# Kernel optimization log

Measured on AMD Instinct MI355X. Metric: run time of the kernel, lower is better.

Reference implementation:

```python
import jax, jax.numpy as jnp
import numpy as np

H = 2048            # hidden_size
INTER = 8192        # intermediate_size
E = 16              # num_experts
V = 32000           # vocab_size
I = INTER // E      # per-expert intermediate (tp_size=1) = 512
N = 4096            # num_tokens
BASE_ROUTING_SCALE = 10.0


def setup_inputs() -> dict:
    key = jax.random.key(0)
    ks = jax.random.split(key, 6)
    x = jax.random.normal(ks[0], (N, H), dtype=jnp.float32)
    token_ids = jax.random.randint(ks[1], (N,), 0, V)
    mu = jax.random.normal(ks[2], (N, H), dtype=jnp.float32)
    # kaiming-uniform-ish scaled params
    gate_up_proj = jax.random.normal(ks[3], (E, H, 2 * I), dtype=jnp.float32) * (1.0 / np.sqrt(H))
    down_proj = jax.random.normal(ks[4], (E, I, H), dtype=jnp.float32) * (1.0 / np.sqrt(I))
    # mu_router initialized to zeros in the module; use small random so routing is actually mu-biased
    mu_router_w = jax.random.normal(ks[5], (E, H), dtype=jnp.float32) * 0.02
    return {"x": x, "token_ids": token_ids, "mu": mu,
            "gate_up_proj": gate_up_proj, "down_proj": down_proj,
            "mu_router_w": mu_router_w}


def reference(x, token_ids, mu, gate_up_proj, down_proj, mu_router_w):
    # --- routing: expert = token_id % E, biased by mu logits ---
    base = jnp.clip(token_ids, 0, V - 1) % E              # [N]
    logits = (jax.nn.one_hot(base, E, dtype=jnp.float32) * BASE_ROUTING_SCALE
              + mu @ mu_router_w.T)                       # [N, E]
    expert_ids = jnp.argmax(logits, axis=-1)              # [N]

    Iloc = gate_up_proj.shape[-1] // 2

    # --- grouped expert SwiGLU MLP: scan over experts, mask-combine outputs ---
    def step(acc, inp):
        wg, wd, e = inp
        gu = x @ wg                                       # [N, 2I]
        h = jax.nn.silu(gu[:, :Iloc]) * gu[:, Iloc:]      # [N, I]
        o = h @ wd                                        # [N, H]
        acc = acc + jnp.where((expert_ids == e)[:, None], o, 0.0)
        return acc, None

    out0 = jnp.zeros_like(x)
    out, _ = jax.lax.scan(step, out0, (gate_up_proj, down_proj, jnp.arange(E)))
    return out
```

## Files before the change

### kernel.cpp

```cpp
#include <hip/hip_runtime.h>
#include <hip/hip_bf16.h>

#define NT 4096
#define HD 2048
#define NE 16
#define ID 512
#define TWO_I 1024
#define PITCH 72
#define MAXITEMS 47

typedef __attribute__((ext_vector_type(8))) short bf16x8_t;
typedef __attribute__((ext_vector_type(4))) float f32x4_t;

__device__ __forceinline__ unsigned short f2bf(float f) {
  union { float f; unsigned int u; } v; v.f = f;
  unsigned int r = v.u + 0x7fffu + ((v.u >> 16) & 1u);
  return (unsigned short)(r >> 16);
}
__device__ __forceinline__ unsigned pk2(unsigned short a, unsigned short b) {
  return (unsigned)a | ((unsigned)b << 16);
}
__device__ __forceinline__ void gl_lds16(const void* g, void* l) {
  __builtin_amdgcn_global_load_lds(
      (const __attribute__((address_space(1))) unsigned int*)g,
      (__attribute__((address_space(3))) unsigned int*)l, 16, 0, 0);
}

__global__ __launch_bounds__(256) void k_prep_gu(const float* __restrict__ gup,
                                                 unsigned short* __restrict__ wgb) {
  int e = blockIdx.y, k0 = blockIdx.x * 32;
  int t = threadIdx.x;
  int cb = t >> 4, c = (t & 15) * 4;
  const float* src = gup + ((size_t)e * HD + k0) * TWO_I + t * 4;
  unsigned short* dst = wgb + (((size_t)e * 16 + cb) * HD + k0) * 64 + c;
#pragma unroll 4
  for (int j = 0; j < 32; ++j) {
    float4 v = *(const float4*)src; src += TWO_I;
    uint2 p; p.x = pk2(f2bf(v.x), f2bf(v.y)); p.y = pk2(f2bf(v.z), f2bf(v.w));
    *(uint2*)dst = p; dst += 64;
  }
}
__global__ __launch_bounds__(256) void k_prep_dn(const float* __restrict__ dwn,
                                                 unsigned short* __restrict__ wdb) {
  int e = blockIdx.y, k0 = blockIdx.x * 32;
  int t = threadIdx.x;
  int cb = t >> 3, c = (t & 7) * 8;
  const float* src = dwn + ((size_t)e * ID + k0) * HD + t * 8;
  unsigned short* dst = wdb + (((size_t)e * 32 + cb) * ID + k0) * 64 + c;
#pragma unroll 4
  for (int j = 0; j < 32; ++j) {
    float4 v0 = *(const float4*)src;
    float4 v1 = *(const float4*)(src + 4); src += HD;
    uint4 p;
    p.x = pk2(f2bf(v0.x), f2bf(v0.y)); p.y = pk2(f2bf(v0.z), f2bf(v0.w));
    p.z = pk2(f2bf(v1.x), f2bf(v1.y)); p.w = pk2(f2bf(v1.z), f2bf(v1.w));
    *(uint4*)dst = p; dst += 64;
  }
}

__global__ void k_cast_x(const float* __restrict__ x, unsigned short* __restrict__ xb) {
  size_t i = ((size_t)blockIdx.x * 256 + threadIdx.x) * 8;
  float4 a = *(const float4*)(x + i);
  float4 b = *(const float4*)(x + i + 4);
  uint4 pk;
  pk.x = pk2(f2bf(a.x), f2bf(a.y)); pk.y = pk2(f2bf(a.z), f2bf(a.w));
  pk.z = pk2(f2bf(b.x), f2bf(b.y)); pk.w = pk2(f2bf(b.z), f2bf(b.w));
  *(uint4*)(xb + i) = pk;
}

__global__ void k_route(const float* __restrict__ mu, const int* __restrict__ tok,
                        const float* __restrict__ wr, int* __restrict__ eid) {
  int t = blockIdx.x;
  int tid = threadIdx.x;
  float p[NE];
#pragma unroll
  for (int e = 0; e < NE; ++e) p[e] = 0.f;
  const float* m = mu + (size_t)t * HD;
  for (int h = tid; h < HD; h += 256) {
    float mv = m[h];
#pragma unroll
    for (int e = 0; e < NE; ++e) p[e] += mv * wr[e * HD + h];
  }
#pragma unroll
  for (int e = 0; e < NE; ++e) {
    float v = p[e];
#pragma unroll
    for (int s = 32; s; s >>= 1) v += __shfl_xor(v, s, 64);
    p[e] = v;
  }
  __shared__ float red[4][NE];
  int lane = tid & 63, wv = tid >> 6;
  if (lane == 0) {
#pragma unroll
    for (int e = 0; e < NE; ++e) red[wv][e] = p[e];
  }
  __syncthreads();
  if (tid == 0) {
    int tk = tok[t];
    if (tk < 0) tk = 0;
    if (tk > 31999) tk = 31999;
    int base = tk & 15;
    float best = -3.0e38f; int bi = 0;
    for (int e = 0; e < NE; ++e) {
      float v = red[0][e] + red[1][e] + red[2][e] + red[3][e];
      if (e == base) v += 10.0f;
      if (v > best) { best = v; bi = e; }
    }
    eid[t] = bi;
  }
}

__global__ void k_init(int* counts, int* cursors) {
  int i = threadIdx.x;
  if (i < NE) { counts[i] = 0; cursors[i] = 0; }
}
__global__ void k_hist(const int* __restrict__ eid, int* __restrict__ counts) {
  int t = blockIdx.x * 256 + threadIdx.x;
  if (t < NT) atomicAdd(&counts[eid[t]], 1);
}
__global__ void k_scan(const int* __restrict__ counts, int* __restrict__ offsets,
                       int* __restrict__ cursors, int* __restrict__ wk) {
  if (threadIdx.x == 0) {
    int s = 0;
    for (int e = 0; e < NE; ++e) { offsets[e] = s; cursors[e] = s; s += counts[e]; }
    offsets[NE] = s;
    int n = 0;
    for (int e = 0; e < NE; ++e) {
      int tiles = (counts[e] + 127) >> 7;
      for (int m = 0; m < tiles; ++m) { wk[n++] = e | (m << 8); }
    }
    wk[MAXITEMS] = n;
  }
}
__global__ void k_scatter(const int* __restrict__ eid, int* __restrict__ cursors,
                          int* __restrict__ tlist) {
  int t = blockIdx.x * 256 + threadIdx.x;
  if (t < NT) {
    int e = eid[t];
    int pos = atomicAdd(&cursors[e], 1);
    tlist[pos] = t;
  }
}

__global__ __launch_bounds__(256, 2) void k_gemm1(
    const unsigned short* __restrict__ xb, const unsigned short* __restrict__ wgb,
    const int* __restrict__ offsets, const int* __restrict__ tlist,
    const int* __restrict__ wk, unsigned short* __restrict__ hbuf) {
  int item = blockIdx.y;
  if (item >= wk[MAXITEMS]) return;
  int w = wk[item];
  int e = w & 255, tb = (w >> 8) * 128;
  int off = offsets[e], cnt = offsets[e + 1] - off;
  int cx = blockIdx.x;
  int c0 = cx * 64;

  __shared__ unsigned short Bb[2][2][64 * 64];
  __shared__ unsigned short Pb[2][128 * PITCH];
  __shared__ int ltok[128];

  int tid = threadIdx.x, lane = tid & 63, wv = tid >> 6;
  if (tid < 128) { int r = tb + tid; if (r > cnt - 1) r = cnt - 1; ltok[tid] = tlist[off + r]; }
  __syncthreads();

  int lr = lane & 15, hi = lane >> 4, mb = wv * 32;
  const unsigned short* aRow0 = xb + (size_t)ltok[mb + lr] * HD + hi * 8;
  const unsigned short* aRow1 = xb + (size_t)ltok[mb + 16 + lr] * HD + hi * 8;

  const unsigned short* gS0;
  const unsigned short* gS1;
  const unsigned short* uS0;
  const unsigned short* uS1;
  {
    const unsigned short* gbase = wgb + ((size_t)(e * 16 + cx) * HD) * 64;
    const unsigned short* ubase = wgb + ((size_t)(e * 16 + 8 + cx) * HD) * 64;
    int lo = lane * 8;
    gS0 = gbase + (wv * 16) * 64 + lo;      gS1 = gbase + (wv * 16 + 8) * 64 + lo;
    uS0 = ubase + (wv * 16) * 64 + lo;      uS1 = ubase + (wv * 16 + 8) * 64 + lo;
  }

#define STAGEB(BUF) do { \
  gl_lds16(gS0, &Bb[BUF][0][(wv * 16) * 64]);     gS0 += 4096; \
  gl_lds16(gS1, &Bb[BUF][0][(wv * 16 + 8) * 64]); gS1 += 4096; \
  gl_lds16(uS0, &Bb[BUF][1][(wv * 16) * 64]);     uS0 += 4096; \
  gl_lds16(uS1, &Bb[BUF][1][(wv * 16 + 8) * 64]); uS1 += 4096; \
} while (0)

  bf16x8_t A0[4], A1[4];
#define LOADA(SET, KT) do { \
  SET[0] = *(const bf16x8_t*)(aRow0 + (KT) * 64); \
  SET[1] = *(const bf16x8_t*)(aRow0 + (KT) * 64 + 32); \
  SET[2] = *(const bf16x8_t*)(aRow1 + (KT) * 64); \
  SET[3] = *(const bf16x8_t*)(aRow1 + (KT) * 64 + 32); \
} while (0)

#define TRANSP(BUF) do { \
  int T_ = lane >> 5, c2_ = (lane & 31) * 2; \
  const unsigned short* b_ = &Bb[BUF][T_][(wv * 16) * 64 + c2_]; \
  unsigned v_[16]; \
  _Pragma("unroll") for (int j = 0; j < 16; ++j) v_[j] = *(const unsigned*)(b_ + j * 64); \
  uint4 lo0_, lo1_, hi0_, hi1_; \
  lo0_.x = (v_[0] & 0xffffu) | (v_[1] << 16);  lo0_.y = (v_[2] & 0xffffu) | (v_[3] << 16); \
  lo0_.z = (v_[4] & 0xffffu) | (v_[5] << 16);  lo0_.w = (v_[6] & 0xffffu) | (v_[7] << 16); \
  lo1_.x = (v_[8] & 0xffffu) | (v_[9] << 16);  lo1_.y = (v_[10] & 0xffffu) | (v_[11] << 16); \
  lo1_.z = (v_[12] & 0xffffu) | (v_[13] << 16); lo1_.w = (v_[14] & 0xffffu) | (v_[15] << 16); \
  hi0_.x = (v_[0] >> 16) | (v_[1] & 0xffff0000u);  hi0_.y = (v_[2] >> 16) | (v_[3] & 0xffff0000u); \
  hi0_.z = (v_[4] >> 16) | (v_[5] & 0xffff0000u);  hi0_.w = (v_[6] >> 16) | (v_[7] & 0xffff0000u); \
  hi1_.x = (v_[8] >> 16) | (v_[9] & 0xffff0000u);  hi1_.y = (v_[10] >> 16) | (v_[11] & 0xffff0000u); \
  hi1_.z = (v_[12] >> 16) | (v_[13] & 0xffff0000u); hi1_.w = (v_[14] >> 16) | (v_[15] & 0xffff0000u); \
  unsigned short* p0_ = &Pb[BUF][(T_ * 64 + c2_) * PITCH + wv * 16]; \
  *(uint4*)p0_ = lo0_; *(uint4*)(p0_ + 8) = lo1_; \
  *(uint4*)(p0_ + PITCH) = hi0_; *(uint4*)(p0_ + PITCH + 8) = hi1_; \
} while (0)

  f32x4_t zero = {0.f, 0.f, 0.f, 0.f};
  f32x4_t accg[2][4], accu[2][4];
#pragma unroll
  for (int m = 0; m < 2; ++m)
#pragma unroll
    for (int n = 0; n < 4; ++n) { accg[m][n] = zero; accu[m][n] = zero; }

#define MFMA_PH(BUF, SET) do { \
  __builtin_amdgcn_s_setprio(1); \
  _Pragma("unroll") for (int kk = 0; kk < 2; ++kk) { \
    int klo = kk * 32 + hi * 8; \
    bf16x8_t a0 = SET[kk], a1 = SET[2 + kk]; \
    _Pragma("unroll") for (int n = 0; n < 4; ++n) { \
      bf16x8_t bg = *(bf16x8_t*)&Pb[BUF][(n * 16 + lr) * PITCH + klo]; \
      bf16x8_t bu = *(bf16x8_t*)&Pb[BUF][(64 + n * 16 + lr) * PITCH + klo]; \
      accg[0][n] = __builtin_amdgcn_mfma_f32_16x16x32_bf16(a0, bg, accg[0][n], 0, 0, 0); \
      accu[0][n] = __builtin_amdgcn_mfma_f32_16x16x32_bf16(a0, bu, accu[0][n], 0, 0, 0); \
      accg[1][n] = __builtin_amdgcn_mfma_f32_16x16x32_bf16(a1, bg, accg[1][n], 0, 0, 0); \
      accu[1][n] = __builtin_amdgcn_mfma_f32_16x16x32_bf16(a1, bu, accu[1][n], 0, 0, 0); \
    } \
  } \
  __builtin_amdgcn_s_setprio(0); \
} while (0)

#define SUBSTEP(KT, BUF, SET, VMC) do { \
  asm volatile("s_waitcnt vmcnt(" #VMC ")" ::: "memory"); \
  __builtin_amdgcn_sched_barrier(0); \
  TRANSP(BUF); \
  asm volatile("s_waitcnt lgkmcnt(0)" ::: "memory"); \
  __builtin_amdgcn_sched_barrier(0); \
  __builtin_amdgcn_s_barrier(); \
  MFMA_PH(BUF, SET); \
  if ((KT) + 2 < 32) { LOADA(SET, (KT) + 2); STAGEB(BUF); } \
} while (0)

  LOADA(A0, 0); STAGEB(0);
  LOADA(A1, 1); STAGEB(1);

  for (int kt2 = 0; kt2 < 15; ++kt2) {
    SUBSTEP(2 * kt2, 0, A0, 8);
    SUBSTEP(2 * kt2 + 1, 1, A1, 8);
  }
  SUBSTEP(30, 0, A0, 8);
  SUBSTEP(31, 1, A1, 0);

#undef SUBSTEP
#undef MFMA_PH
#undef TRANSP
#undef LOADA
#undef STAGEB

  int rq = hi * 4;
#pragma unroll
  for (int m = 0; m < 2; ++m)
#pragma unroll
    for (int n = 0; n < 4; ++n)
#pragma unroll
      for (int j = 0; j < 4; ++j) {
        int r = tb + mb + m * 16 + rq + j;
        if (r < cnt) {
          float g = accg[m][n][j], u = accu[m][n][j];
          float hv = (g / (1.f + __expf(-g))) * u;
          hbuf[(size_t)(off + r) * ID + c0 + n * 16 + lr] = f2bf(hv);
        }
      }
}

__global__ __launch_bounds__(256, 2) void k_gemm2(
    const unsigned short* __restrict__ hbuf, const unsigned short* __restrict__ wdb,
    const int* __restrict__ offsets, const int* __restrict__ tlist,
    const int* __restrict__ wk, float* __restrict__ out) {
  int item = blockIdx.y;
  if (item >= wk[MAXITEMS]) return;
  int w = wk[item];
  int e = w & 255, tb = (w >> 8) * 128;
  int off = offsets[e], cnt = offsets[e + 1] - off;
  int cx = blockIdx.x;
  int c0 = cx * 128;

  __shared__ unsigned short Bb[2][2][64 * 64];
  __shared__ unsigned short Pb[2][128 * PITCH];

  int tid = threadIdx.x, lane = tid & 63, wv = tid >> 6;
  int lr = lane & 15, hi = lane >> 4, mb = wv * 32;

  int r0 = tb + mb + lr;      if (r0 > cnt - 1) r0 = cnt - 1;
  int r1 = tb + mb + 16 + lr; if (r1 > cnt - 1) r1 = cnt - 1;
  const unsigned short* aRow0 = hbuf + (size_t)(off + r0) * ID + hi * 8;
  const unsigned short* aRow1 = hbuf + (size_t)(off + r1) * ID + hi * 8;

  const unsigned short* gS0;
  const unsigned short* gS1;
  const unsigned short* uS0;
  const unsigned short* uS1;
  {
    const unsigned short* b0 = wdb + ((size_t)(e * 32 + 2 * cx) * ID) * 64;
    const unsigned short* b1 = wdb + ((size_t)(e * 32 + 2 * cx + 1) * ID) * 64;
    int lo = lane * 8;
    gS0 = b0 + (wv * 16) * 64 + lo;  gS1 = b0 + (wv * 16 + 8) * 64 + lo;
    uS0 = b1 + (wv * 16) * 64 + lo;  uS1 = b1 + (wv * 16 + 8) * 64 + lo;
  }

#define STAGEB(BUF) do { \
  gl_lds16(gS0, &Bb[BUF][0][(wv * 16) * 64]);     gS0 += 4096; \
  gl_lds16(gS1, &Bb[BUF][0][(wv * 16 + 8) * 64]); gS1 += 4096; \
  gl_lds16(uS0, &Bb[BUF][1][(wv * 16) * 64]);     uS0 += 4096; \
  gl_lds16(uS1, &Bb[BUF][1][(wv * 16 + 8) * 64]); uS1 += 4096; \
} while (0)

  bf16x8_t A0[4], A1[4];
#define LOADA(SET, KT) do { \
  SET[0] = *(const bf16x8_t*)(aRow0 + (KT) * 64); \
  SET[1] = *(const bf16x8_t*)(aRow0 + (KT) * 64 + 32); \
  SET[2] = *(const bf16x8_t*)(aRow1 + (KT) * 64); \
  SET[3] = *(const bf16x8_t*)(aRow1 + (KT) * 64 + 32); \
} while (0)

#define TRANSP(BUF) do { \
  int T_ = lane >> 5, c2_ = (lane & 31) * 2; \
  const unsigned short* b_ = &Bb[BUF][T_][(wv * 16) * 64 + c2_]; \
  unsigned v_[16]; \
  _Pragma("unroll") for (int j = 0; j < 16; ++j) v_[j] = *(const unsigned*)(b_ + j * 64); \
  uint4 lo0_, lo1_, hi0_, hi1_; \
  lo0_.x = (v_[0] & 0xffffu) | (v_[1] << 16);  lo0_.y = (v_[2] & 0xffffu) | (v_[3] << 16); \
  lo0_.z = (v_[4] & 0xffffu) | (v_[5] << 16);  lo0_.w = (v_[6] & 0xffffu) | (v_[7] << 16); \
  lo1_.x = (v_[8] & 0xffffu) | (v_[9] << 16);  lo1_.y = (v_[10] & 0xffffu) | (v_[11] << 16); \
  lo1_.z = (v_[12] & 0xffffu) | (v_[13] << 16); lo1_.w = (v_[14] & 0xffffu) | (v_[15] << 16); \
  hi0_.x = (v_[0] >> 16) | (v_[1] & 0xffff0000u);  hi0_.y = (v_[2] >> 16) | (v_[3] & 0xffff0000u); \
  hi0_.z = (v_[4] >> 16) | (v_[5] & 0xffff0000u);  hi0_.w = (v_[6] >> 16) | (v_[7] & 0xffff0000u); \
  hi1_.x = (v_[8] >> 16) | (v_[9] & 0xffff0000u);  hi1_.y = (v_[10] >> 16) | (v_[11] & 0xffff0000u); \
  hi1_.z = (v_[12] >> 16) | (v_[13] & 0xffff0000u); hi1_.w = (v_[14] >> 16) | (v_[15] & 0xffff0000u); \
  unsigned short* p0_ = &Pb[BUF][(T_ * 64 + c2_) * PITCH + wv * 16]; \
  *(uint4*)p0_ = lo0_; *(uint4*)(p0_ + 8) = lo1_; \
  *(uint4*)(p0_ + PITCH) = hi0_; *(uint4*)(p0_ + PITCH + 8) = hi1_; \
} while (0)

  f32x4_t zero = {0.f, 0.f, 0.f, 0.f};
  f32x4_t acc[2][8];
#pragma unroll
  for (int m = 0; m < 2; ++m)
#pragma unroll
    for (int n = 0; n < 8; ++n) acc[m][n] = zero;

#define MFMA_PH(BUF, SET) do { \
  __builtin_amdgcn_s_setprio(1); \
  _Pragma("unroll") for (int kk = 0; kk < 2; ++kk) { \
    int klo = kk * 32 + hi * 8; \
    bf16x8_t a0 = SET[kk], a1 = SET[2 + kk]; \
    _Pragma("unroll") for (int n = 0; n < 8; ++n) { \
      bf16x8_t b = *(bf16x8_t*)&Pb[BUF][(n * 16 + lr) * PITCH + klo]; \
      acc[0][n] = __builtin_amdgcn_mfma_f32_16x16x32_bf16(a0, b, acc[0][n], 0, 0, 0); \
      acc[1][n] = __builtin_amdgcn_mfma_f32_16x16x32_bf16(a1, b, acc[1][n], 0, 0, 0); \
    } \
  } \
  __builtin_amdgcn_s_setprio(0); \
} while (0)

#define SUBSTEP(KT, BUF, SET, VMC) do { \
  asm volatile("s_waitcnt vmcnt(" #VMC ")" ::: "memory"); \
  __builtin_amdgcn_sched_barrier(0); \
  TRANSP(BUF); \
  asm volatile("s_waitcnt lgkmcnt(0)" ::: "memory"); \
  __builtin_amdgcn_sched_barrier(0); \
  __builtin_amdgcn_s_barrier(); \
  MFMA_PH(BUF, SET); \
  if ((KT) + 2 < 8) { LOADA(SET, (KT) + 2); STAGEB(BUF); } \
} while (0)

  LOADA(A0, 0); STAGEB(0);
  LOADA(A1, 1); STAGEB(1);

  SUBSTEP(0, 0, A0, 8);
  SUBSTEP(1, 1, A1, 8);
  SUBSTEP(2, 0, A0, 8);
  SUBSTEP(3, 1, A1, 8);
  SUBSTEP(4, 0, A0, 8);
  SUBSTEP(5, 1, A1, 8);
  SUBSTEP(6, 0, A0, 8);
  SUBSTEP(7, 1, A1, 0);

#undef SUBSTEP
#undef MFMA_PH
#undef TRANSP
#undef LOADA
#undef STAGEB

  int rq = hi * 4;
#pragma unroll
  for (int m = 0; m < 2; ++m)
#pragma unroll
    for (int n = 0; n < 8; ++n)
#pragma unroll
      for (int j = 0; j < 4; ++j) {
        int r = tb + mb + m * 16 + rq + j;
        if (r < cnt) {
          out[(size_t)tlist[off + r] * HD + c0 + n * 16 + lr] = acc[m][n][j];
        }
      }
}

extern "C" void kernel_launch(void* const* d_in, const int* in_sizes, int n_in,
                              void* d_out, int out_size, void* d_ws, size_t ws_size,
                              hipStream_t stream) {
  (void)in_sizes; (void)n_in; (void)out_size; (void)ws_size;
  const float* x   = (const float*)d_in[0];
  const int*   tok = (const int*)d_in[1];
  const float* mu  = (const float*)d_in[2];
  const float* gup = (const float*)d_in[3];
  const float* dwn = (const float*)d_in[4];
  const float* wr  = (const float*)d_in[5];
  float* out = (float*)d_out;

  char* ws = (char*)d_ws;
  int* eid     = (int*)ws;
  int* tlist   = (int*)(ws + 16384);
  int* counts  = (int*)(ws + 32768);
  int* offsets = (int*)(ws + 32896);
  int* cursors = (int*)(ws + 33024);
  int* wk      = (int*)(ws + 33152);
  unsigned short* xb   = (unsigned short*)(ws + 65536);
  unsigned short* hbuf = (unsigned short*)(ws + 65536 + 16777216);
  unsigned short* wgb  = (unsigned short*)(ws + 65536 + 16777216 + 4194304);
  unsigned short* wdb  = (unsigned short*)(ws + 65536 + 16777216 + 4194304 + 67108864);

  k_prep_gu<<<dim3(64, 16), 256, 0, stream>>>(gup, wgb);
  k_prep_dn<<<dim3(16, 16), 256, 0, stream>>>(dwn, wdb);
  k_cast_x <<<4096, 256, 0, stream>>>(x, xb);
  k_route  <<<NT, 256, 0, stream>>>(mu, tok, wr, eid);
  k_init   <<<1, 64, 0, stream>>>(counts, cursors);
  k_hist   <<<16, 256, 0, stream>>>(eid, counts);
  k_scan   <<<1, 64, 0, stream>>>(counts, offsets, cursors, wk);
  k_scatter<<<16, 256, 0, stream>>>(eid, cursors, tlist);
  k_gemm1  <<<dim3(8, MAXITEMS), 256, 0, stream>>>(xb, wgb, offsets, tlist, wk, hbuf);
  k_gemm2  <<<dim3(16, MAXITEMS), 256, 0, stream>>>(hbuf, wdb, offsets, tlist, wk, out);
}
```

Measured before the change: 234.3 us.

## Pre-transpose and XOR-swizzle weights in prep kernels; deepen GEMM pipeline to four stages

The weight prep kernels now transpose each 64x64 bf16 tile through shared memory and store it in an XOR-swizzled, MFMA-ready layout. The GEMM kernels therefore no longer run a per-iteration LDS transpose pass with its extra LDS traffic and lgkmcnt wait. Both GEMMs also move from double to quad buffering, prefetching three k-tiles ahead with four register sets for A. The cost is more LDS per block, which may limit occupancy, and a prep kernel that now synchronizes on shared memory.

```diff
diff --git a/kernel.cpp b/kernel.cpp
--- a/kernel.cpp
+++ b/kernel.cpp
@@ -6,7 +6,6 @@
 #define NE 16
 #define ID 512
 #define TWO_I 1024
-#define PITCH 72
 #define MAXITEMS 47
 
 typedef __attribute__((ext_vector_type(8))) short bf16x8_t;
@@ -28,33 +27,70 @@
 
 __global__ __launch_bounds__(256) void k_prep_gu(const float* __restrict__ gup,
                                                  unsigned short* __restrict__ wgb) {
-  int e = blockIdx.y, k0 = blockIdx.x * 32;
-  int t = threadIdx.x;
-  int cb = t >> 4, c = (t & 15) * 4;
-  const float* src = gup + ((size_t)e * HD + k0) * TWO_I + t * 4;
-  unsigned short* dst = wgb + (((size_t)e * 16 + cb) * HD + k0) * 64 + c;
-#pragma unroll 4
-  for (int j = 0; j < 32; ++j) {
-    float4 v = *(const float4*)src; src += TWO_I;
-    uint2 p; p.x = pk2(f2bf(v.x), f2bf(v.y)); p.y = pk2(f2bf(v.z), f2bf(v.w));
-    *(uint2*)dst = p; dst += 64;
+  int kt = blockIdx.x, e = blockIdx.y;
+  int K0 = kt * 64;
+  int t = threadIdx.x, w = t >> 6, lane = t & 63;
+  __shared__ unsigned short L[64][264];
+  for (int q = 0; q < 4; ++q) {
+    for (int rd = 0; rd < 16; ++rd) {
+      int row = rd * 4 + w;
+      const float* s = gup + ((size_t)e * HD + K0 + row) * TWO_I + q * 256 + lane * 4;
+      float4 v = *(const float4*)s;
+      uint2 p; p.x = pk2(f2bf(v.x), f2bf(v.y)); p.y = pk2(f2bf(v.z), f2bf(v.w));
+      *(uint2*)&L[row][lane * 4] = p;
+    }
+    __syncthreads();
+    int cbl = (t >> 5) & 3, c = (t & 31) * 2, kh = t >> 7;
+    int cb = q * 4 + cbl;
+    unsigned short* tb = wgb + (((size_t)e * 16 + cb) * 32 + kt) * 4096;
+    int cc = cbl * 64 + c;
+    for (int j = kh * 4; j < kh * 4 + 4; ++j) {
+      unsigned vv[8];
+#pragma unroll
+      for (int i = 0; i < 8; ++i) vv[i] = *(const unsigned*)&L[j * 8 + i][cc];
+      uint4 lo, hi2;
+      lo.x = (vv[0] & 0xffffu) | (vv[1] << 16);  lo.y = (vv[2] & 0xffffu) | (vv[3] << 16);
+      lo.z = (vv[4] & 0xffffu) | (vv[5] << 16);  lo.w = (vv[6] & 0xffffu) | (vv[7] << 16);
+      hi2.x = (vv[0] >> 16) | (vv[1] & 0xffff0000u);  hi2.y = (vv[2] >> 16) | (vv[3] & 0xffff0000u);
+      hi2.z = (vv[4] >> 16) | (vv[5] & 0xffff0000u);  hi2.w = (vv[6] >> 16) | (vv[7] & 0xffff0000u);
+      *(uint4*)&tb[c * 64 + ((j ^ (c & 7)) * 8)] = lo;
+      *(uint4*)&tb[(c + 1) * 64 + ((j ^ ((c + 1) & 7)) * 8)] = hi2;
+    }
+    __syncthreads();
   }
 }
 __global__ __launch_bounds__(256) void k_prep_dn(const float* __restrict__ dwn,
                                                  unsigned short* __restrict__ wdb) {
-  int e = blockIdx.y, k0 = blockIdx.x * 32;
-  int t = threadIdx.x;
-  int cb = t >> 3, c = (t & 7) * 8;
-  const float* src = dwn + ((size_t)e * ID + k0) * HD + t * 8;
-  unsigned short* dst = wdb + (((size_t)e * 32 + cb) * ID + k0) * 64 + c;
-#pragma unroll 4
-  for (int j = 0; j < 32; ++j) {
-    float4 v0 = *(const float4*)src;
-    float4 v1 = *(const float4*)(src + 4); src += HD;
-    uint4 p;
-    p.x = pk2(f2bf(v0.x), f2bf(v0.y)); p.y = pk2(f2bf(v0.z), f2bf(v0.w));
-    p.z = pk2(f2bf(v1.x), f2bf(v1.y)); p.w = pk2(f2bf(v1.z), f2bf(v1.w));
-    *(uint4*)dst = p; dst += 64;
+  int kt = blockIdx.x, e = blockIdx.y, half = blockIdx.z;
+  int K0 = kt * 64;
+  int t = threadIdx.x, w = t >> 6, lane = t & 63;
+  __shared__ unsigned short L[64][264];
+  for (int q = 0; q < 4; ++q) {
+    for (int rd = 0; rd < 16; ++rd) {
+      int row = rd * 4 + w;
+      const float* s = dwn + ((size_t)e * ID + K0 + row) * HD + half * 1024 + q * 256 + lane * 4;
+      float4 v = *(const float4*)s;
+      uint2 p; p.x = pk2(f2bf(v.x), f2bf(v.y)); p.y = pk2(f2bf(v.z), f2bf(v.w));
+      *(uint2*)&L[row][lane * 4] = p;
+    }
+    __syncthreads();
+    int cbl = (t >> 5) & 3, c = (t & 31) * 2, kh = t >> 7;
+    int cb = half * 16 + q * 4 + cbl;
+    unsigned short* tb = wdb + (((size_t)e * 32 + cb) * 8 + kt) * 4096;
+    int cc = cbl * 64 + c;
+    for (int j = kh * 4; j < kh * 4 + 4; ++j) {
+      unsigned vv[8];
+#pragma unroll
+      for (int i = 0; i < 8; ++i) vv[i] = *(const unsigned*)&L[j * 8 + i][cc];
+      uint4 lo, hi2;
+      lo.x = (vv[0] & 0xffffu) | (vv[1] << 16);  lo.y = (vv[2] & 0xffffu) | (vv[3] << 16);
+      lo.z = (vv[4] & 0xffffu) | (vv[5] << 16);  lo.w = (vv[6] & 0xffffu) | (vv[7] << 16);
+      hi2.x = (vv[0] >> 16) | (vv[1] & 0xffff0000u);  hi2.y = (vv[2] >> 16) | (vv[3] & 0xffff0000u);
+      hi2.z = (vv[4] >> 16) | (vv[5] & 0xffff0000u);  hi2.w = (vv[6] >> 16) | (vv[7] & 0xffff0000u);
+      *(uint4*)&tb[c * 64 + ((j ^ (c & 7)) * 8)] = lo;
+      *(uint4*)&tb[(c + 1) * 64 + ((j ^ ((c + 1) & 7)) * 8)] = hi2;
+    }
+    __syncthreads();
   }
 }
 
@@ -154,8 +190,7 @@
   int cx = blockIdx.x;
   int c0 = cx * 64;
 
-  __shared__ unsigned short Bb[2][2][64 * 64];
-  __shared__ unsigned short Pb[2][128 * PITCH];
+  __shared__ unsigned short Pb[4][2][4096];
   __shared__ int ltok[128];
 
   int tid = threadIdx.x, lane = tid & 63, wv = tid >> 6;
@@ -166,51 +201,23 @@
   const unsigned short* aRow0 = xb + (size_t)ltok[mb + lr] * HD + hi * 8;
   const unsigned short* aRow1 = xb + (size_t)ltok[mb + 16 + lr] * HD + hi * 8;
 
-  const unsigned short* gS0;
-  const unsigned short* gS1;
-  const unsigned short* uS0;
-  const unsigned short* uS1;
-  {
-    const unsigned short* gbase = wgb + ((size_t)(e * 16 + cx) * HD) * 64;
-    const unsigned short* ubase = wgb + ((size_t)(e * 16 + 8 + cx) * HD) * 64;
-    int lo = lane * 8;
-    gS0 = gbase + (wv * 16) * 64 + lo;      gS1 = gbase + (wv * 16 + 8) * 64 + lo;
-    uS0 = ubase + (wv * 16) * 64 + lo;      uS1 = ubase + (wv * 16 + 8) * 64 + lo;
-  }
+  int gu = wv >> 1, part = wv & 1;
+  const unsigned short* wS =
+      wgb + (((size_t)e * 16 + (gu ? 8 + cx : cx)) * 32) * 4096 + part * 2048 + lane * 8;
 
 #define STAGEB(BUF) do { \
-  gl_lds16(gS0, &Bb[BUF][0][(wv * 16) * 64]);     gS0 += 4096; \
-  gl_lds16(gS1, &Bb[BUF][0][(wv * 16 + 8) * 64]); gS1 += 4096; \
-  gl_lds16(uS0, &Bb[BUF][1][(wv * 16) * 64]);     uS0 += 4096; \
-  gl_lds16(uS1, &Bb[BUF][1][(wv * 16 + 8) * 64]); uS1 += 4096; \
-} while (0)
-
-  bf16x8_t A0[4], A1[4];
+  gl_lds16(wS,        &Pb[BUF][gu][part * 2048]); \
+  gl_lds16(wS + 512,  &Pb[BUF][gu][part * 2048 + 512]); \
+  gl_lds16(wS + 1024, &Pb[BUF][gu][part * 2048 + 1024]); \
+  gl_lds16(wS + 1536, &Pb[BUF][gu][part * 2048 + 1536]); \
+  wS += 4096; } while (0)
+
+  bf16x8_t A0[4], A1[4], A2[4], A3[4];
 #define LOADA(SET, KT) do { \
   SET[0] = *(const bf16x8_t*)(aRow0 + (KT) * 64); \
   SET[1] = *(const bf16x8_t*)(aRow0 + (KT) * 64 + 32); \
   SET[2] = *(const bf16x8_t*)(aRow1 + (KT) * 64); \
-  SET[3] = *(const bf16x8_t*)(aRow1 + (KT) * 64 + 32); \
-} while (0)
-
-#define TRANSP(BUF) do { \
-  int T_ = lane >> 5, c2_ = (lane & 31) * 2; \
-  const unsigned short* b_ = &Bb[BUF][T_][(wv * 16) * 64 + c2_]; \
-  unsigned v_[16]; \
-  _Pragma("unroll") for (int j = 0; j < 16; ++j) v_[j] = *(const unsigned*)(b_ + j * 64); \
-  uint4 lo0_, lo1_, hi0_, hi1_; \
-  lo0_.x = (v_[0] & 0xffffu) | (v_[1] << 16);  lo0_.y = (v_[2] & 0xffffu) | (v_[3] << 16); \
-  lo0_.z = (v_[4] & 0xffffu) | (v_[5] << 16);  lo0_.w = (v_[6] & 0xffffu) | (v_[7] << 16); \
-  lo1_.x = (v_[8] & 0xffffu) | (v_[9] << 16);  lo1_.y = (v_[10] & 0xffffu) | (v_[11] << 16); \
-  lo1_.z = (v_[12] & 0xffffu) | (v_[13] << 16); lo1_.w = (v_[14] & 0xffffu) | (v_[15] << 16); \
-  hi0_.x = (v_[0] >> 16) | (v_[1] & 0xffff0000u);  hi0_.y = (v_[2] >> 16) | (v_[3] & 0xffff0000u); \
-  hi0_.z = (v_[4] >> 16) | (v_[5] & 0xffff0000u);  hi0_.w = (v_[6] >> 16) | (v_[7] & 0xffff0000u); \
-  hi1_.x = (v_[8] >> 16) | (v_[9] & 0xffff0000u);  hi1_.y = (v_[10] >> 16) | (v_[11] & 0xffff0000u); \
-  hi1_.z = (v_[12] >> 16) | (v_[13] & 0xffff0000u); hi1_.w = (v_[14] >> 16) | (v_[15] & 0xffff0000u); \
-  unsigned short* p0_ = &Pb[BUF][(T_ * 64 + c2_) * PITCH + wv * 16]; \
-  *(uint4*)p0_ = lo0_; *(uint4*)(p0_ + 8) = lo1_; \
-  *(uint4*)(p0_ + PITCH) = hi0_; *(uint4*)(p0_ + PITCH + 8) = hi1_; \
-} while (0)
+  SET[3] = *(const bf16x8_t*)(aRow1 + (KT) * 64 + 32); } while (0)
 
   f32x4_t zero = {0.f, 0.f, 0.f, 0.f};
   f32x4_t accg[2][4], accu[2][4];
@@ -222,44 +229,46 @@
 #define MFMA_PH(BUF, SET) do { \
   __builtin_amdgcn_s_setprio(1); \
   _Pragma("unroll") for (int kk = 0; kk < 2; ++kk) { \
-    int klo = kk * 32 + hi * 8; \
+    int cidx = kk * 4 + hi; \
     bf16x8_t a0 = SET[kk], a1 = SET[2 + kk]; \
     _Pragma("unroll") for (int n = 0; n < 4; ++n) { \
-      bf16x8_t bg = *(bf16x8_t*)&Pb[BUF][(n * 16 + lr) * PITCH + klo]; \
-      bf16x8_t bu = *(bf16x8_t*)&Pb[BUF][(64 + n * 16 + lr) * PITCH + klo]; \
+      int r = n * 16 + lr; \
+      int o = r * 64 + ((cidx ^ (r & 7)) * 8); \
+      bf16x8_t bg = *(bf16x8_t*)&Pb[BUF][0][o]; \
+      bf16x8_t bu = *(bf16x8_t*)&Pb[BUF][1][o]; \
       accg[0][n] = __builtin_amdgcn_mfma_f32_16x16x32_bf16(a0, bg, accg[0][n], 0, 0, 0); \
       accu[0][n] = __builtin_amdgcn_mfma_f32_16x16x32_bf16(a0, bu, accu[0][n], 0, 0, 0); \
       accg[1][n] = __builtin_amdgcn_mfma_f32_16x16x32_bf16(a1, bg, accg[1][n], 0, 0, 0); \
       accu[1][n] = __builtin_amdgcn_mfma_f32_16x16x32_bf16(a1, bu, accu[1][n], 0, 0, 0); \
-    } \
-  } \
-  __builtin_amdgcn_s_setprio(0); \
-} while (0)
-
-#define SUBSTEP(KT, BUF, SET, VMC) do { \
+    } } \
+  __builtin_amdgcn_s_setprio(0); } while (0)
+
+#define SUBSTEP(KT, BUF, SETC, SETN, VMC) do { \
   asm volatile("s_waitcnt vmcnt(" #VMC ")" ::: "memory"); \
   __builtin_amdgcn_sched_barrier(0); \
-  TRANSP(BUF); \
-  asm volatile("s_waitcnt lgkmcnt(0)" ::: "memory"); \
-  __builtin_amdgcn_sched_barrier(0); \
   __builtin_amdgcn_s_barrier(); \
-  MFMA_PH(BUF, SET); \
-  if ((KT) + 2 < 32) { LOADA(SET, (KT) + 2); STAGEB(BUF); } \
+  MFMA_PH(BUF, SETC); \
+  if ((KT) + 3 < 32) { LOADA(SETN, (KT) + 3); STAGEB(((BUF) + 3) & 3); } \
 } while (0)
 
   LOADA(A0, 0); STAGEB(0);
   LOADA(A1, 1); STAGEB(1);
-
-  for (int kt2 = 0; kt2 < 15; ++kt2) {
-    SUBSTEP(2 * kt2, 0, A0, 8);
-    SUBSTEP(2 * kt2 + 1, 1, A1, 8);
-  }
-  SUBSTEP(30, 0, A0, 8);
-  SUBSTEP(31, 1, A1, 0);
+  LOADA(A2, 2); STAGEB(2);
+
+  for (int g = 0; g < 7; ++g) {
+    int k4 = g * 4;
+    SUBSTEP(k4 + 0, 0, A0, A3, 16);
+    SUBSTEP(k4 + 1, 1, A1, A0, 16);
+    SUBSTEP(k4 + 2, 2, A2, A1, 16);
+    SUBSTEP(k4 + 3, 3, A3, A2, 16);
+  }
+  SUBSTEP(28, 0, A0, A3, 16);
+  SUBSTEP(29, 1, A1, A0, 16);
+  SUBSTEP(30, 2, A2, A1, 8);
+  SUBSTEP(31, 3, A3, A2, 0);
 
 #undef SUBSTEP
 #undef MFMA_PH
-#undef TRANSP
 #undef LOADA
 #undef STAGEB
 
@@ -291,8 +300,7 @@
   int cx = blockIdx.x;
   int c0 = cx * 128;
 
-  __shared__ unsigned short Bb[2][2][64 * 64];
-  __shared__ unsigned short Pb[2][128 * PITCH];
+  __shared__ unsigned short Pb[4][2][4096];
 
   int tid = threadIdx.x, lane = tid & 63, wv = tid >> 6;
   int lr = lane & 15, hi = lane >> 4, mb = wv * 32;
@@ -302,51 +310,23 @@
   const unsigned short* aRow0 = hbuf + (size_t)(off + r0) * ID + hi * 8;
   const unsigned short* aRow1 = hbuf + (size_t)(off + r1) * ID + hi * 8;
 
-  const unsigned short* gS0;
-  const unsigned short* gS1;
-  const unsigned short* uS0;
-  const unsigned short* uS1;
-  {
-    const unsigned short* b0 = wdb + ((size_t)(e * 32 + 2 * cx) * ID) * 64;
-    const unsigned short* b1 = wdb + ((size_t)(e * 32 + 2 * cx + 1) * ID) * 64;
-    int lo = lane * 8;
-    gS0 = b0 + (wv * 16) * 64 + lo;  gS1 = b0 + (wv * 16 + 8) * 64 + lo;
-    uS0 = b1 + (wv * 16) * 64 + lo;  uS1 = b1 + (wv * 16 + 8) * 64 + lo;
-  }
+  int gu = wv >> 1, part = wv & 1;
+  const unsigned short* wS =
+      wdb + (((size_t)e * 32 + 2 * cx + gu) * 8) * 4096 + part * 2048 + lane * 8;
 
 #define STAGEB(BUF) do { \
-  gl_lds16(gS0, &Bb[BUF][0][(wv * 16) * 64]);     gS0 += 4096; \
-  gl_lds16(gS1, &Bb[BUF][0][(wv * 16 + 8) * 64]); gS1 += 4096; \
-  gl_lds16(uS0, &Bb[BUF][1][(wv * 16) * 64]);     uS0 += 4096; \
-  gl_lds16(uS1, &Bb[BUF][1][(wv * 16 + 8) * 64]); uS1 += 4096; \
-} while (0)
-
-  bf16x8_t A0[4], A1[4];
+  gl_lds16(wS,        &Pb[BUF][gu][part * 2048]); \
+  gl_lds16(wS + 512,  &Pb[BUF][gu][part * 2048 + 512]); \
+  gl_lds16(wS + 1024, &Pb[BUF][gu][part * 2048 + 1024]); \
+  gl_lds16(wS + 1536, &Pb[BUF][gu][part * 2048 + 1536]); \
+  wS += 4096; } while (0)
+
+  bf16x8_t A0[4], A1[4], A2[4], A3[4];
 #define LOADA(SET, KT) do { \
   SET[0] = *(const bf16x8_t*)(aRow0 + (KT) * 64); \
   SET[1] = *(const bf16x8_t*)(aRow0 + (KT) * 64 + 32); \
   SET[2] = *(const bf16x8_t*)(aRow1 + (KT) * 64); \
-  SET[3] = *(const bf16x8_t*)(aRow1 + (KT) * 64 + 32); \
-} while (0)
-
-#define TRANSP(BUF) do { \
-  int T_ = lane >> 5, c2_ = (lane & 31) * 2; \
-  const unsigned short* b_ = &Bb[BUF][T_][(wv * 16) * 64 + c2_]; \
-  unsigned v_[16]; \
-  _Pragma("unroll") for (int j = 0; j < 16; ++j) v_[j] = *(const unsigned*)(b_ + j * 64); \
-  uint4 lo0_, lo1_, hi0_, hi1_; \
-  lo0_.x = (v_[0] & 0xffffu) | (v_[1] << 16);  lo0_.y = (v_[2] & 0xffffu) | (v_[3] << 16); \
-  lo0_.z = (v_[4] & 0xffffu) | (v_[5] << 16);  lo0_.w = (v_[6] & 0xffffu) | (v_[7] << 16); \
-  lo1_.x = (v_[8] & 0xffffu) | (v_[9] << 16);  lo1_.y = (v_[10] & 0xffffu) | (v_[11] << 16); \
-  lo1_.z = (v_[12] & 0xffffu) | (v_[13] << 16); lo1_.w = (v_[14] & 0xffffu) | (v_[15] << 16); \
-  hi0_.x = (v_[0] >> 16) | (v_[1] & 0xffff0000u);  hi0_.y = (v_[2] >> 16) | (v_[3] & 0xffff0000u); \
-  hi0_.z = (v_[4] >> 16) | (v_[5] & 0xffff0000u);  hi0_.w = (v_[6] >> 16) | (v_[7] & 0xffff0000u); \
-  hi1_.x = (v_[8] >> 16) | (v_[9] & 0xffff0000u);  hi1_.y = (v_[10] >> 16) | (v_[11] & 0xffff0000u); \
-  hi1_.z = (v_[12] >> 16) | (v_[13] & 0xffff0000u); hi1_.w = (v_[14] >> 16) | (v_[15] & 0xffff0000u); \
-  unsigned short* p0_ = &Pb[BUF][(T_ * 64 + c2_) * PITCH + wv * 16]; \
-  *(uint4*)p0_ = lo0_; *(uint4*)(p0_ + 8) = lo1_; \
-  *(uint4*)(p0_ + PITCH) = hi0_; *(uint4*)(p0_ + PITCH + 8) = hi1_; \
-} while (0)
+  SET[3] = *(const bf16x8_t*)(aRow1 + (KT) * 64 + 32); } while (0)
 
   f32x4_t zero = {0.f, 0.f, 0.f, 0.f};
   f32x4_t acc[2][8];
@@ -358,43 +338,40 @@
 #define MFMA_PH(BUF, SET) do { \
   __builtin_amdgcn_s_setprio(1); \
   _Pragma("unroll") for (int kk = 0; kk < 2; ++kk) { \
-    int klo = kk * 32 + hi * 8; \
+    int cidx = kk * 4 + hi; \
     bf16x8_t a0 = SET[kk], a1 = SET[2 + kk]; \
     _Pragma("unroll") for (int n = 0; n < 8; ++n) { \
-      bf16x8_t b = *(bf16x8_t*)&Pb[BUF][(n * 16 + lr) * PITCH + klo]; \
+      int r = (n & 3) * 16 + lr; \
+      int o = r * 64 + ((cidx ^ (r & 7)) * 8); \
+      bf16x8_t b = *(bf16x8_t*)&Pb[BUF][n >> 2][o]; \
       acc[0][n] = __builtin_amdgcn_mfma_f32_16x16x32_bf16(a0, b, acc[0][n], 0, 0, 0); \
       acc[1][n] = __builtin_amdgcn_mfma_f32_16x16x32_bf16(a1, b, acc[1][n], 0, 0, 0); \
-    } \
-  } \
-  __builtin_amdgcn_s_setprio(0); \
-} while (0)
-
-#define SUBSTEP(KT, BUF, SET, VMC) do { \
+    } } \
+  __builtin_amdgcn_s_setprio(0); } while (0)
+
+#define SUBSTEP(KT, BUF, SETC, SETN, VMC) do { \
   asm volatile("s_waitcnt vmcnt(" #VMC ")" ::: "memory"); \
   __builtin_amdgcn_sched_barrier(0); \
-  TRANSP(BUF); \
-  asm volatile("s_waitcnt lgkmcnt(0)" ::: "memory"); \
-  __builtin_amdgcn_sched_barrier(0); \
   __builtin_amdgcn_s_barrier(); \
-  MFMA_PH(BUF, SET); \
-  if ((KT) + 2 < 8) { LOADA(SET, (KT) + 2); STAGEB(BUF); } \
+  MFMA_PH(BUF, SETC); \
+  if ((KT) + 3 < 8) { LOADA(SETN, (KT) + 3); STAGEB(((BUF) + 3) & 3); } \
 } while (0)
 
   LOADA(A0, 0); STAGEB(0);
   LOADA(A1, 1); STAGEB(1);
-
-  SUBSTEP(0, 0, A0, 8);
-  SUBSTEP(1, 1, A1, 8);
-  SUBSTEP(2, 0, A0, 8);
-  SUBSTEP(3, 1, A1, 8);
-  SUBSTEP(4, 0, A0, 8);
-  SUBSTEP(5, 1, A1, 8);
-  SUBSTEP(6, 0, A0, 8);
-  SUBSTEP(7, 1, A1, 0);
+  LOADA(A2, 2); STAGEB(2);
+
+  SUBSTEP(0, 0, A0, A3, 16);
+  SUBSTEP(1, 1, A1, A0, 16);
+  SUBSTEP(2, 2, A2, A1, 16);
+  SUBSTEP(3, 3, A3, A2, 16);
+  SUBSTEP(4, 0, A0, A3, 16);
+  SUBSTEP(5, 1, A1, A0, 16);
+  SUBSTEP(6, 2, A2, A1, 8);
+  SUBSTEP(7, 3, A3, A2, 0);
 
 #undef SUBSTEP
 #undef MFMA_PH
-#undef TRANSP
 #undef LOADA
 #undef STAGEB
 
@@ -436,8 +413,8 @@
   unsigned short* wgb  = (unsigned short*)(ws + 65536 + 16777216 + 4194304);
   unsigned short* wdb  = (unsigned short*)(ws + 65536 + 16777216 + 4194304 + 67108864);
 
-  k_prep_gu<<<dim3(64, 16), 256, 0, stream>>>(gup, wgb);
-  k_prep_dn<<<dim3(16, 16), 256, 0, stream>>>(dwn, wdb);
+  k_prep_gu<<<dim3(32, 16), 256, 0, stream>>>(gup, wgb);
+  k_prep_dn<<<dim3(8, 16, 2), 256, 0, stream>>>(dwn, wdb);
   k_cast_x <<<4096, 256, 0, stream>>>(x, xb);
   k_route  <<<NT, 256, 0, stream>>>(mu, tok, wr, eid);
   k_init   <<<1, 64, 0, stream>>>(counts, cursors);
```

Result: no change. 231.5 us (-1.2%).
